# Kernel tuning notes

Measured on AMD Instinct MI355X. Metric: run time of the kernel, lower is better.

## Reference

```python
import jax, jax.numpy as jnp
import numpy as np

NFMODES = 512   # spinful lattice: 2 * 256 sites
NE = 256        # number of occupied fermion modes per configuration
NUNPAIRED = 32
NMODES = NFMODES - NUNPAIRED
BATCH = 32


def slogpf(A):
    """(sign, log|Pf|) of an even-dim antisymmetric matrix via Parlett-Reid
    LTL^T elimination with partial pivoting (pfapack pfaffian_LTL algorithm)."""
    n = A.shape[0]
    ar = jnp.arange(n)
    one = jnp.asarray(1.0, A.dtype)
    zero = jnp.asarray(0.0, A.dtype)

    def step(carry, k):
        A, sign, logabs = carry
        # pivot row: argmax |A[k+1:, k]|
        m1 = ar > k
        kp = jnp.argmax(jnp.where(m1, jnp.abs(A[:, k]), -one))
        # swap rows and columns k+1 <-> kp (Pf flips sign on a swap)
        perm = ar.at[k + 1].set(kp).at[kp].set(k + 1)
        A = A[perm][:, perm]
        sign = jnp.where(kp != k + 1, -sign, sign)
        pivot = A[k, k + 1]  # Pf *= A[k, k+1]
        sign = sign * jnp.sign(pivot)
        logabs = logabs + jnp.log(jnp.abs(pivot))
        # rank-2 update of the trailing submatrix A[k+2:, k+2:]
        m2 = ar > (k + 1)
        tau = jnp.where(m2, A[k, :] / pivot, zero)  # A[k, k+2:] / A[k, k+1]
        c = jnp.where(m2, A[:, k + 1], zero)        # A[k+2:, k+1]
        A = A + jnp.outer(tau, c) - jnp.outer(c, tau)
        return (A, sign, logabs), None

    ks = jnp.arange(0, n - 1, 2)
    (_, sign, logabs), _ = jax.lax.scan(step, (A, one, zero), ks)
    return sign, logabs


def setup_inputs() -> dict:
    key = jax.random.key(0)
    k1, k2, k3 = jax.random.split(key, 3)
    U = jax.random.normal(k1, (NFMODES, NFMODES), jnp.float32)
    # equal-pairing diagonal init (as in the module) + noise for nontrivial pivoting
    diag = jnp.diag(jnp.tile(jnp.array([1.0, 0.0], jnp.float32), NMODES // 2)[:-1], k=1)
    J = diag + 0.1 * jax.random.normal(k2, (NMODES, NMODES), jnp.float32)
    # occupied-mode indices: NE unique sorted indices per sample (fermion_idx output)
    idx = jax.vmap(lambda k: jnp.sort(jax.random.permutation(k, NFMODES)[:NE]))(
        jax.random.split(k3, BATCH)).astype(jnp.int32)
    return {"U": U, "J": J, "idx": idx, "Nunpaired": NUNPAIRED}


def reference(U, J, idx, Nunpaired):
    Ja = (J - J.T) / 2  # enforce antisymmetry of the pairing matrix

    def single(ix):
        Usel = U[ix]                      # [NE, NFMODES] gather of occupied rows
        Uun = Usel[:, :Nunpaired]         # [NE, Nunpaired] unpaired orbitals
        Up = Usel[:, Nunpaired:]          # [NE, NMODES]   paired orbitals
        F = Up @ Ja @ Up.T                # [NE, NE] antisymmetric pairing block
        O = jnp.zeros((Nunpaired, Nunpaired), F.dtype)
        Ffull = jnp.block([[F, Uun], [-Uun.T, O]])  # [NE+Nun, NE+Nun]
        return slogpf(Ffull)

    sign, logabs = jax.vmap(single)(idx)
    return sign, logabs
```

## Files before the change

### kernel.cpp

```cpp
#include <hip/hip_runtime.h>
#include <hip/hip_bf16.h>
#include <math.h>

#define NFM 512
#define NE  256
#define NUN 32
#define NM  480
#define NB  32
#define NF  288
#define WP  16
#define PAIRS 8
#define PP  18
#define THETA 0.03125f

typedef unsigned long long ull;

__global__ __launch_bounds__(256)
void build_ja_k(const float* __restrict__ J, float* __restrict__ Ja) {
  int t = blockIdx.x * blockDim.x + threadIdx.x;
  int stride = gridDim.x * blockDim.x;
  for (int e = t; e < NM * NM; e += stride) {
    int i = e / NM, j = e - i * NM;
    Ja[e] = 0.5f * (J[i * NM + j] - J[j * NM + i]);
  }
}

__global__ __launch_bounds__(256)
void gemm1_k(const float* __restrict__ U, const int* __restrict__ idx,
             const float* __restrict__ Ja, float* __restrict__ Tmp) {
  const int b  = blockIdx.z;
  const int m0 = blockIdx.y << 6;
  const int n0 = blockIdx.x << 6;
  const int tid = threadIdx.x;
  __shared__ float As[16][64];
  __shared__ float Bs[16][64];
  const int ar = tid >> 2, ac = (tid & 3) << 2;
  const int br = tid >> 4, bc = (tid & 15) << 2;
  const int tx = tid & 15, ty = tid >> 4;
  const float* Arow = U + (size_t)idx[b * NE + m0 + ar] * NFM + NUN;
  float acc[4][4] = {};
  for (int l0 = 0; l0 < NM; l0 += 16) {
    float4 av = *(const float4*)(Arow + l0 + ac);
    As[ac + 0][ar] = av.x; As[ac + 1][ar] = av.y;
    As[ac + 2][ar] = av.z; As[ac + 3][ar] = av.w;
    float4 bv = make_float4(0.f, 0.f, 0.f, 0.f);
    if (n0 + bc < NM) bv = *(const float4*)(Ja + (size_t)(l0 + br) * NM + n0 + bc);
    *(float4*)(&Bs[br][bc]) = bv;
    __syncthreads();
#pragma unroll
    for (int kk = 0; kk < 16; ++kk) {
      float4 a4 = *(const float4*)(&As[kk][ty << 2]);
      float4 b4 = *(const float4*)(&Bs[kk][tx << 2]);
      float a[4] = {a4.x, a4.y, a4.z, a4.w};
      float bb[4] = {b4.x, b4.y, b4.z, b4.w};
#pragma unroll
      for (int q = 0; q < 4; ++q)
#pragma unroll
        for (int p = 0; p < 4; ++p) acc[q][p] = fmaf(a[q], bb[p], acc[q][p]);
    }
    __syncthreads();
  }
  float* Tb = Tmp + (size_t)b * NE * NM;
#pragma unroll
  for (int q = 0; q < 4; ++q) {
    int r = m0 + (ty << 2) + q;
#pragma unroll
    for (int p = 0; p < 4; ++p) {
      int m = n0 + (tx << 2) + p;
      if (m < NM) Tb[(size_t)r * NM + m] = acc[q][p];
    }
  }
}

__global__ __launch_bounds__(256)
void gemm2_k(const float* __restrict__ U, const int* __restrict__ idx,
             const float* __restrict__ Tmp, float* __restrict__ Ff) {
  const int b  = blockIdx.z;
  const int m0 = blockIdx.y << 6;
  const int n0 = blockIdx.x << 6;
  const int tid = threadIdx.x;
  __shared__ float As[16][64];
  __shared__ float Bs[16][64];
  const int ar = tid >> 2, ac = (tid & 3) << 2;
  const int jr = tid >> 2, kc = (tid & 3) << 2;
  const int tx = tid & 15, ty = tid >> 4;
  const float* Arow = Tmp + ((size_t)b * NE + m0 + ar) * NM;
  const float* Brow = U + (size_t)idx[b * NE + n0 + jr] * NFM + NUN;
  float acc[4][4] = {};
  for (int l0 = 0; l0 < NM; l0 += 16) {
    float4 av = *(const float4*)(Arow + l0 + ac);
    As[ac + 0][ar] = av.x; As[ac + 1][ar] = av.y;
    As[ac + 2][ar] = av.z; As[ac + 3][ar] = av.w;
    float4 bv = *(const float4*)(Brow + l0 + kc);
    Bs[kc + 0][jr] = bv.x; Bs[kc + 1][jr] = bv.y;
    Bs[kc + 2][jr] = bv.z; Bs[kc + 3][jr] = bv.w;
    __syncthreads();
#pragma unroll
    for (int kk = 0; kk < 16; ++kk) {
      float4 a4 = *(const float4*)(&As[kk][ty << 2]);
      float4 b4 = *(const float4*)(&Bs[kk][tx << 2]);
      float a[4] = {a4.x, a4.y, a4.z, a4.w};
      float bb[4] = {b4.x, b4.y, b4.z, b4.w};
#pragma unroll
      for (int q = 0; q < 4; ++q)
#pragma unroll
        for (int p = 0; p < 4; ++p) acc[q][p] = fmaf(a[q], bb[p], acc[q][p]);
    }
    __syncthreads();
  }
  float* Fb = Ff + (size_t)b * NF * NF;
#pragma unroll
  for (int q = 0; q < 4; ++q) {
    int i = m0 + (ty << 2) + q;
#pragma unroll
    for (int p = 0; p < 4; ++p) {
      int j = n0 + (tx << 2) + p;
      Fb[(size_t)i * NF + j] = acc[q][p];
    }
  }
}

__global__ __launch_bounds__(256)
void fill_edges_k(const float* __restrict__ U, const int* __restrict__ idx,
                  float* __restrict__ Ff) {
  const int b = blockIdx.x;
  const int tid = threadIdx.x;
  float* Fb = Ff + (size_t)b * NF * NF;
  const int gr = idx[b * NE + tid];
#pragma unroll 4
  for (int u = 0; u < NUN; ++u) {
    float v = U[(size_t)gr * NFM + u];
    Fb[(size_t)tid * NF + NE + u] = v;
    Fb[(size_t)(NE + u) * NF + tid] = -v;
  }
  if (tid < NUN) {
    for (int v = 0; v < NUN; ++v) Fb[(size_t)(NE + tid) * NF + NE + v] = 0.f;
  }
}

__global__ __launch_bounds__(512)
void pfpanel_k(float* __restrict__ Ff, float* __restrict__ out) {
  const int b = blockIdx.x;
  float* __restrict__ A = Ff + (size_t)b * NF * NF;
  const int tid = threadIdx.x;
  __shared__ __align__(16) float P[NF * PP];
  __shared__ __align__(16) float2 s_tc[PAIRS][NF];
  __shared__ __align__(16) float s_colbuf[NF];
  __shared__ float s_oldrow[WP];
  __shared__ float s_pivdef[2];
  __shared__ float s_invp[PAIRS];
  __shared__ __align__(16) unsigned s_redu[2][8];

  float sign = 1.f, logabs = 0.f;

#pragma unroll 1
  for (int k0 = 0; k0 < NF; k0 += WP) {
    const int pend = k0 + WP;

    if (k0 == 0) {
      for (int e = tid; e < NF * 4; e += 512) {
        int r = e >> 2, c4 = (e & 3) << 2;
        float4 v = *(const float4*)(A + (size_t)r * NF + c4);
        float2* d = (float2*)&P[r * PP + c4];
        d[0] = make_float2(v.x, v.y);
        d[1] = make_float2(v.z, v.w);
      }
      __syncthreads();
    }

#pragma unroll 1
    for (int mp = 0; mp < PAIRS; ++mp) {
      const int k = k0 + 2 * mp, lc = 2 * mp, lc1 = lc + 1;
      const int par = mp & 1;

      float vk = 0.f, vk1 = 0.f;
      unsigned pk = 0;
      if (tid > k && tid < NF) {
        float2 pv = *(const float2*)&P[tid * PP + lc];
        vk = pv.x; vk1 = pv.y;
#pragma unroll
        for (int m = 0; m < PAIRS - 1; ++m) {
          float2 ti  = s_tc[m][tid];
          float2 tk  = s_tc[m][k];
          float2 tk1 = s_tc[m][k + 1];
          float im = s_invp[m];
          float d0 = im * (ti.x * tk.y  - ti.y * tk.x);
          float d1 = im * (ti.x * tk1.y - ti.y * tk1.x);
          vk  += (m < mp) ? d0 : 0.f;
          vk1 += (m < mp) ? d1 : 0.f;
        }
        s_colbuf[tid] = vk;
        if (tid > k + 1) s_tc[mp][tid] = make_float2(-vk, vk1);
        else             s_pivdef[par] = vk;
        pk = (__float_as_uint(fabsf(vk)) & 0xFFFFFE00u) | (unsigned)tid;
      }
#pragma unroll
      for (int s = 32; s > 0; s >>= 1) {
        unsigned o = (unsigned)__shfl_xor((int)pk, s, 64);
        if (o > pk) pk = o;
      }
      if ((tid & 63) == 0) s_redu[par][tid >> 6] = pk;
      __syncthreads();
      uint4 r0 = *(const uint4*)&s_redu[par][0];
      uint4 r1 = *(const uint4*)&s_redu[par][4];
      unsigned best = r0.x;
      best = best > r0.y ? best : r0.y;
      best = best > r0.z ? best : r0.z;
      best = best > r0.w ? best : r0.w;
      best = best > r1.x ? best : r1.x;
      best = best > r1.y ? best : r1.y;
      best = best > r1.z ? best : r1.z;
      best = best > r1.w ? best : r1.w;
      const float vmax = __uint_as_float(best & 0xFFFFFE00u);
      const float pivdef = -s_pivdef[par];
      const bool doswap = fabsf(pivdef) < THETA * vmax;

      if (!doswap) {
        const float invp = 1.f / pivdef;
        s_invp[mp] = invp;
        if (tid == 0) {
          sign *= (pivdef > 0.f ? 1.f : (pivdef < 0.f ? -1.f : 0.f));
          logabs += logf(fabsf(pivdef));
        }
      } else {
        const int kp = (int)(best & 0x1FFu);
        const float pivot = -s_colbuf[kp];
        const float invp = 1.f / pivot;
        s_invp[mp] = invp;
        if (tid == 0) {
          sign = -sign;
          sign *= (pivot > 0.f ? 1.f : (pivot < 0.f ? -1.f : 0.f));
          logabs += logf(fabsf(pivot));
        }
        const bool inpanel = (kp < pend);
        float gvr = 0.f;
        if (inpanel) {
          const int lckp = kp - k0;
          if (tid > k + 1 && tid < NF && tid != kp) {
            float a = P[tid * PP + lc1], b2 = P[tid * PP + lckp];
            P[tid * PP + lc1] = b2; P[tid * PP + lckp] = a;
          } else if (tid >= NF && tid < NF + WP) {
            int c = tid - NF;
            if (c != lc1 && c != lckp) {
              float a = P[(k + 1) * PP + c], b2 = P[kp * PP + c];
              P[(k + 1) * PP + c] = b2; P[kp * PP + c] = a;
            }
          } else if (tid == NF + WP) {
            float a = P[kp * PP + lc1];
            float b2 = P[(k + 1) * PP + lckp];
            P[(k + 1) * PP + lc1] = 0.f;  P[(k + 1) * PP + lckp] = a;
            P[kp * PP + lc1] = b2;        P[kp * PP + lckp] = 0.f;
          } else if (tid >= NF + 24 && tid < NF + 24 + mp) {
            int m = tid - (NF + 24);
            float2 a = s_tc[m][k + 1], b2 = s_tc[m][kp];
            s_tc[m][k + 1] = b2; s_tc[m][kp] = a;
          }
        } else {
          if (tid >= pend && tid < NF) {
            if (tid == kp) {
              A[(size_t)kp * NF + kp] = 0.f;
            } else {
              float pvv = P[tid * PP + lc1];
              gvr = A[(size_t)tid * NF + kp];
              A[(size_t)tid * NF + kp] = pvv;
              A[(size_t)kp * NF + tid] = -pvv;
            }
          } else if (tid >= NF && tid < NF + WP) {
            int c = tid - NF;
            float old = P[kp * PP + c];
            s_oldrow[c] = old;
            P[kp * PP + c] = P[(k + 1) * PP + c];
          } else if (tid >= NF + 24 && tid < NF + 24 + mp) {
            int m = tid - (NF + 24);
            float2 a = s_tc[m][k + 1], b2 = s_tc[m][kp];
            s_tc[m][k + 1] = b2; s_tc[m][kp] = a;
          }
        }
        __syncthreads();
        if (tid > k + 1 && tid < NF) {
          float vpost = (tid == kp) ? s_colbuf[k + 1] : vk;
          float cc;
          if (inpanel)        cc = P[tid * PP + lc1];
          else if (tid < pend) cc = -s_oldrow[tid - k0];
          else if (tid == kp)  cc = -s_oldrow[lc1];
          else                 cc = gvr;
#pragma unroll 1
          for (int m = 0; m < mp; ++m) {
            const float im = s_invp[m];
            float2 ti = s_tc[m][tid], tk1 = s_tc[m][k + 1];
            cc = fmaf(ti.x, im * tk1.y, fmaf(-ti.y, im * tk1.x, cc));
          }
          s_tc[mp][tid] = make_float2(-vpost, cc);
        }
        __syncthreads();
      }
    }
    __syncthreads();

    if (pend < NF) {
      const int ty = tid >> 6, tx = tid & 63;
      const int nch = (NF - pend) >> 2;
      float ivr[PAIRS];
#pragma unroll
      for (int m = 0; m < PAIRS; ++m) ivr[m] = s_invp[m];
      for (int jb = 0; jb < nch; jb += 64) {
        const int j4 = jb + tx;
        if (j4 < nch) {
          const int j = pend + (j4 << 2);
          const bool stageP = (j4 < (WP >> 2));
          float4 tj[PAIRS], cj[PAIRS];
#pragma unroll
          for (int m = 0; m < PAIRS; ++m) {
            const float im = ivr[m];
            float4 q0 = *(const float4*)(&s_tc[m][j]);
            float4 q1 = *(const float4*)(&s_tc[m][j + 2]);
            tj[m] = make_float4(q0.x * im, q0.z * im, q1.x * im, q1.z * im);
            cj[m] = make_float4(q0.y * im, q0.w * im, q1.y * im, q1.w * im);
          }
#pragma unroll 2
          for (int i = pend + ty; i < NF; i += 8) {
            float* ap = A + (size_t)i * NF + j;
            float4 a = *(float4*)ap;
#pragma unroll
            for (int m = 0; m < PAIRS; ++m) {
              const float2 t = s_tc[m][i];
              a.x = fmaf(t.x, cj[m].x, fmaf(-t.y, tj[m].x, a.x));
              a.y = fmaf(t.x, cj[m].y, fmaf(-t.y, tj[m].y, a.y));
              a.z = fmaf(t.x, cj[m].z, fmaf(-t.y, tj[m].z, a.z));
              a.w = fmaf(t.x, cj[m].w, fmaf(-t.y, tj[m].w, a.w));
            }
            *(float4*)ap = a;
            if (stageP) {
              float2* d = (float2*)&P[i * PP + (j - pend)];
              d[0] = make_float2(a.x, a.y);
              d[1] = make_float2(a.z, a.w);
            }
          }
        }
      }
    }
    __syncthreads();
  }

  if (tid == 0) { out[b] = sign; out[NB + b] = logabs; }
}

extern "C" void kernel_launch(void* const* d_in, const int* in_sizes, int n_in,
                              void* d_out, int out_size, void* d_ws, size_t ws_size,
                              hipStream_t stream) {
  const float* U  = (const float*)d_in[0];
  const float* J  = (const float*)d_in[1];
  const int* idx  = (const int*)d_in[2];
  float* out = (float*)d_out;
  float* ws = (float*)d_ws;

  float* Ja  = ws;
  float* Tmp = Ja + (size_t)NM * NM;
  float* Ff  = Tmp + (size_t)NB * NE * NM;

  build_ja_k<<<dim3(256), dim3(256), 0, stream>>>(J, Ja);
  gemm1_k<<<dim3(8, 4, NB), dim3(256), 0, stream>>>(U, idx, Ja, Tmp);
  gemm2_k<<<dim3(4, 4, NB), dim3(256), 0, stream>>>(U, idx, Tmp, Ff);
  fill_edges_k<<<dim3(NB), dim3(256), 0, stream>>>(U, idx, Ff);
  pfpanel_k<<<dim3(NB), dim3(512), 0, stream>>>(Ff, out);
}
```

Baseline: 354.0 us.

## Precompute U·Ja once for all rows and exploit antisymmetry in F gemm

The first GEMM now computes W = U_paired · Ja once for all 512 rows, not per-sample on gathered rows, so the batch dimension drops out of that stage. The second GEMM gathers rows of W by idx and computes only the lower-triangular tiles of F, writing each result and its negated transpose. This cuts first-stage FLOPs and nearly halves second-stage work. The cost is strided mirrored stores and some idle blocks that return early. It relies on F being exactly antisymmetric, which holds mathematically but is no longer computed independently for both halves.

After: 331.5 us. -6.3%, faster.

```diff
diff --git a/kernel.cpp b/kernel.cpp
--- a/kernel.cpp
+++ b/kernel.cpp
@@ -26,9 +26,8 @@
 }
 
 __global__ __launch_bounds__(256)
-void gemm1_k(const float* __restrict__ U, const int* __restrict__ idx,
-             const float* __restrict__ Ja, float* __restrict__ Tmp) {
-  const int b  = blockIdx.z;
+void gemm_w_k(const float* __restrict__ U, const float* __restrict__ Ja,
+              float* __restrict__ W) {
   const int m0 = blockIdx.y << 6;
   const int n0 = blockIdx.x << 6;
   const int tid = threadIdx.x;
@@ -37,7 +36,7 @@
   const int ar = tid >> 2, ac = (tid & 3) << 2;
   const int br = tid >> 4, bc = (tid & 15) << 2;
   const int tx = tid & 15, ty = tid >> 4;
-  const float* Arow = U + (size_t)idx[b * NE + m0 + ar] * NFM + NUN;
+  const float* Arow = U + (size_t)(m0 + ar) * NFM + NUN;
   float acc[4][4] = {};
   for (int l0 = 0; l0 < NM; l0 += 16) {
     float4 av = *(const float4*)(Arow + l0 + ac);
@@ -60,31 +59,32 @@
     }
     __syncthreads();
   }
-  float* Tb = Tmp + (size_t)b * NE * NM;
 #pragma unroll
   for (int q = 0; q < 4; ++q) {
     int r = m0 + (ty << 2) + q;
 #pragma unroll
     for (int p = 0; p < 4; ++p) {
       int m = n0 + (tx << 2) + p;
-      if (m < NM) Tb[(size_t)r * NM + m] = acc[q][p];
+      if (m < NM) W[(size_t)r * NM + m] = acc[q][p];
     }
   }
 }
 
 __global__ __launch_bounds__(256)
 void gemm2_k(const float* __restrict__ U, const int* __restrict__ idx,
-             const float* __restrict__ Tmp, float* __restrict__ Ff) {
+             const float* __restrict__ W, float* __restrict__ Ff) {
   const int b  = blockIdx.z;
-  const int m0 = blockIdx.y << 6;
-  const int n0 = blockIdx.x << 6;
+  const int by = blockIdx.y, bx = blockIdx.x;
+  if (by < bx) return;
+  const int m0 = by << 6;
+  const int n0 = bx << 6;
   const int tid = threadIdx.x;
   __shared__ float As[16][64];
   __shared__ float Bs[16][64];
   const int ar = tid >> 2, ac = (tid & 3) << 2;
   const int jr = tid >> 2, kc = (tid & 3) << 2;
   const int tx = tid & 15, ty = tid >> 4;
-  const float* Arow = Tmp + ((size_t)b * NE + m0 + ar) * NM;
+  const float* Arow = W + (size_t)idx[b * NE + m0 + ar] * NM;
   const float* Brow = U + (size_t)idx[b * NE + n0 + jr] * NFM + NUN;
   float acc[4][4] = {};
   for (int l0 = 0; l0 < NM; l0 += 16) {
@@ -109,6 +109,7 @@
     __syncthreads();
   }
   float* Fb = Ff + (size_t)b * NF * NF;
+  const bool mirror = (by > bx);
 #pragma unroll
   for (int q = 0; q < 4; ++q) {
     int i = m0 + (ty << 2) + q;
@@ -116,6 +117,7 @@
     for (int p = 0; p < 4; ++p) {
       int j = n0 + (tx << 2) + p;
       Fb[(size_t)i * NF + j] = acc[q][p];
+      if (mirror) Fb[(size_t)j * NF + i] = -acc[q][p];
     }
   }
 }
@@ -354,13 +356,13 @@
   float* out = (float*)d_out;
   float* ws = (float*)d_ws;
 
-  float* Ja  = ws;
-  float* Tmp = Ja + (size_t)NM * NM;
-  float* Ff  = Tmp + (size_t)NB * NE * NM;
+  float* Ja = ws;
+  float* W  = Ja + (size_t)NM * NM;
+  float* Ff = W + (size_t)NFM * NM;
 
   build_ja_k<<<dim3(256), dim3(256), 0, stream>>>(J, Ja);
-  gemm1_k<<<dim3(8, 4, NB), dim3(256), 0, stream>>>(U, idx, Ja, Tmp);
-  gemm2_k<<<dim3(4, 4, NB), dim3(256), 0, stream>>>(U, idx, Tmp, Ff);
+  gemm_w_k<<<dim3(8, 8), dim3(256), 0, stream>>>(U, Ja, W);
+  gemm2_k<<<dim3(4, 4, NB), dim3(256), 0, stream>>>(U, idx, W, Ff);
   fill_edges_k<<<dim3(NB), dim3(256), 0, stream>>>(U, idx, Ff);
   pfpanel_k<<<dim3(NB), dim3(512), 0, stream>>>(Ff, out);
 }
```
